# Kernel tuning notes

Hardware: AMD Instinct MI355X
Metric: run time of the kernel (lower is better)

The kernel has to match this reference:

```python
import jax, jax.numpy as jnp
import numpy as np

PE_DIM = 64

def _layernorm(x, g, b, eps=1e-5):
    m = jnp.mean(x, -1, keepdims=True)
    v = jnp.mean((x - m) ** 2, -1, keepdims=True)
    return (x - m) * jax.lax.rsqrt(v + eps) * g + b

def _sinusoidal_pe(t, dim=PE_DIM):
    half = dim // 2
    freqs = jnp.exp(-jnp.log(10000.0) * jnp.arange(half) / half).astype(t.dtype)
    ang = t[..., None] * freqs  # [..., half]
    return jnp.concatenate([jnp.sin(ang), jnp.cos(ang)], -1)

def _bilinear(feats, b, t, x, y):
    # feats [B,Wl,H,W,D]; b,t int32 [B,Q,Wl,M] (b broadcastable); x,y in [0,1]
    # matches torch grid_sample(mode=bilinear, padding_mode=border, align_corners=False)
    H, W = feats.shape[2], feats.shape[3]
    px = x * W - 0.5
    py = y * H - 0.5
    x0 = jnp.floor(px); y0 = jnp.floor(py)
    wx = (px - x0)[..., None]; wy = (py - y0)[..., None]
    x0i = jnp.clip(x0.astype(jnp.int32), 0, W - 1)
    x1i = jnp.clip(x0.astype(jnp.int32) + 1, 0, W - 1)
    y0i = jnp.clip(y0.astype(jnp.int32), 0, H - 1)
    y1i = jnp.clip(y0.astype(jnp.int32) + 1, 0, H - 1)
    v00 = feats[b, t, y0i, x0i]  # [B,Q,Wl,M,D]
    v01 = feats[b, t, y0i, x1i]
    v10 = feats[b, t, y1i, x0i]
    v11 = feats[b, t, y1i, x1i]
    return (v00 * (1 - wy) * (1 - wx) + v01 * (1 - wy) * wx
            + v10 * wy * (1 - wx) + v11 * wy * wx)

def setup_inputs() -> dict:
    key = jax.random.key(0)
    ks = jax.random.split(key, 20)
    B, Q, Wl, H, W, D, M = 4, 300, 8, 64, 64, 256, 4
    s = 0.02
    inp = {
        'q': jax.random.normal(ks[0], (B, Q, D), jnp.float32),
        'kv_feats': jax.random.normal(ks[1], (B, Wl, H, W, D), jnp.float32),
        'kv_mask': jnp.zeros((B, Wl, H, W), jnp.bool_),
        'delta_sec': jax.random.normal(ks[2], (B, Q, Wl), jnp.float32),
        'w_ref': jax.random.normal(ks[3], (D, 2), jnp.float32) * s,
        'b_ref': jnp.zeros((2,), jnp.float32),
        'w_delta': jax.random.normal(ks[4], (2 * D, 3 * M), jnp.float32) * s,
        'b_delta': jnp.zeros((3 * M,), jnp.float32),
        'w_alpha': jax.random.normal(ks[5], (2 * D, M), jnp.float32) * s,
        'b_alpha': jnp.zeros((M,), jnp.float32),
        'lam': jnp.array(1.0, jnp.float32),
        'w_proj': jax.random.normal(ks[6], (D, D), jnp.float32) * s,
        'b_proj': jnp.zeros((D,), jnp.float32),
        'ln1_g': jnp.ones((D,), jnp.float32), 'ln1_b': jnp.zeros((D,), jnp.float32),
        'ln2_g': jnp.ones((D,), jnp.float32), 'ln2_b': jnp.zeros((D,), jnp.float32),
        'w_ffn1': jax.random.normal(ks[7], (D, 4 * D), jnp.float32) * s,
        'b_ffn1': jnp.zeros((4 * D,), jnp.float32),
        'w_ffn2': jax.random.normal(ks[8], (4 * D, D), jnp.float32) * s,
        'b_ffn2': jnp.zeros((D,), jnp.float32),
        'w_rel': jax.random.normal(ks[9], (PE_DIM, D), jnp.float32) * s,
        'b_rel': jnp.zeros((D,), jnp.float32),
    }
    return inp

def reference(q, kv_feats, kv_mask, delta_sec, w_ref, b_ref, w_delta, b_delta,
              w_alpha, b_alpha, lam, w_proj, b_proj, ln1_g, ln1_b, ln2_g, ln2_b,
              w_ffn1, b_ffn1, w_ffn2, b_ffn2, w_rel, b_rel):
    B, Q, D = q.shape
    Wl = kv_feats.shape[1]
    M = w_alpha.shape[1]

    qn = _layernorm(q, ln1_g, ln1_b)
    rel_feat = _sinusoidal_pe(delta_sec) @ w_rel + b_rel          # [B,Q,Wl,D]
    psi = jnp.concatenate([jnp.broadcast_to(qn[:, :, None, :], (B, Q, Wl, D)),
                           rel_feat], -1)                          # [B,Q,Wl,2D]

    delta = (psi @ w_delta + b_delta).reshape(B, Q, Wl, M, 3)
    logits = psi @ w_alpha + b_alpha                               # [B,Q,Wl,M]
    ref = jax.nn.sigmoid(qn @ w_ref + b_ref)                       # [B,Q,2]
    coords = ref[:, :, None, None, :] + jnp.tanh(delta[..., :2])   # [B,Q,Wl,M,2]
    coords = jnp.clip(coords, 0.0, 1.0)
    delta_t = jnp.tanh(delta[..., 2])                              # [B,Q,Wl,M]

    # mask features (mask==True -> invalid -> zero)
    feats = kv_feats * (~kv_mask)[..., None].astype(kv_feats.dtype)

    # temporal trilinear indices
    base = jnp.arange(Wl, dtype=q.dtype).reshape(1, 1, Wl, 1)
    target = base + delta_t
    t0f = jnp.clip(jnp.floor(target), 0, Wl - 1)
    t1f = jnp.clip(t0f + 1, 0, Wl - 1)
    alpha = (target - t0f)[..., None]
    t0 = t0f.astype(jnp.int32); t1 = t1f.astype(jnp.int32)

    bidx = jnp.arange(B, dtype=jnp.int32).reshape(B, 1, 1, 1)
    cx = coords[..., 0]; cy = coords[..., 1]
    s0 = _bilinear(feats, bidx, t0, cx, cy)                        # [B,Q,Wl,M,D]
    s1 = _bilinear(feats, bidx, t1, cx, cy)
    sampled = s0 * (1 - alpha) + s1 * alpha

    lam_sp = jax.nn.softplus(lam)
    weights = jax.nn.softmax(logits - lam_sp * jnp.abs(delta_sec)[..., None], axis=-1)
    agg = jnp.sum(weights[..., None] * sampled, axis=(2, 3))       # [B,Q,D]

    out = q + (agg @ w_proj + b_proj)
    h = _layernorm(out, ln2_g, ln2_b)
    ffn = jax.nn.gelu(h @ w_ffn1 + b_ffn1, approximate=False) @ w_ffn2 + b_ffn2
    return out + ffn
```

## Files before the change

kernel.cpp:

```cpp
#include <hip/hip_runtime.h>
#include <math.h>

#define Bn 4
#define Qn 300
#define WL 8
#define Hh 64
#define Ww 64
#define Dd 256
#define Mm 4

__device__ __forceinline__ float wave_reduce(float v) {
#pragma unroll
    for (int off = 32; off > 0; off >>= 1) v += __shfl_down(v, off, 64);
    return v;
}

using h2_t = _Float16 __attribute__((ext_vector_type(2)));

__device__ __forceinline__ unsigned packh2(float a, float b) {
    auto h = __builtin_amdgcn_cvt_pkrtz(a, b);
    union { decltype(h) h; unsigned u; } x; x.h = h; return x.u;
}

__device__ __forceinline__ h2_t u2h2(unsigned u) {
    union { unsigned u; h2_t h; } x; x.u = u; return x.h;
}

__device__ __forceinline__ float dot2p(unsigned a, unsigned w, float acc) {
#if __has_builtin(__builtin_amdgcn_fdot2)
    return __builtin_amdgcn_fdot2(u2h2(a), u2h2(w), acc, false);
#else
    h2_t A = u2h2(a), W = u2h2(w);
    return acc + (float)A.x * (float)W.x + (float)A.y * (float)W.y;
#endif
}

__device__ __forceinline__ float dot8h(uint4 av, uint4 wv, float acc) {
    acc = dot2p(av.x, wv.x, acc);
    acc = dot2p(av.y, wv.y, acc);
    acc = dot2p(av.z, wv.z, acc);
    acc = dot2p(av.w, wv.w, acc);
    return acc;
}

__global__ void __launch_bounds__(512, 4) k_front(const float* __restrict__ wp,
                                                  const float* __restrict__ wf1,
                                                  const float* __restrict__ wf2,
                                                  unsigned* __restrict__ pk,
                                                  const float* __restrict__ q,
                                                  const float* __restrict__ g1,
                                                  const float* __restrict__ b1,
                                                  const float* __restrict__ w_ref,
                                                  const float* __restrict__ b_ref,
                                                  const float* __restrict__ dsec,
                                                  const float* __restrict__ w_rel,
                                                  const float* __restrict__ b_rel,
                                                  const float* __restrict__ w_delta,
                                                  const float* __restrict__ b_delta,
                                                  const float* __restrict__ w_alpha,
                                                  const float* __restrict__ b_alpha,
                                                  const unsigned char* __restrict__ mask,
                                                  const float* __restrict__ feats,
                                                  float* __restrict__ agg) {
    int bid = blockIdx.x, t = threadIdx.x;

    if (bid < 576) {
        int i = bid * 512 + t;
        if (i < 32768) {
            int p = i & 3, c = (i >> 2) & 255, g = i >> 10;
            pk[i] = packh2(wp[(g * 8 + 2 * p) * 256 + c], wp[(g * 8 + 2 * p + 1) * 256 + c]);
        } else if (i < 163840) {
            int i2 = i - 32768;
            int p = i2 & 3, c = (i2 >> 2) & 1023, g = i2 >> 12;
            pk[i] = packh2(wf1[(g * 8 + 2 * p) * 1024 + c], wf1[(g * 8 + 2 * p + 1) * 1024 + c]);
        } else {
            int i3 = i - 163840;
            int p = i3 & 3, c = (i3 >> 2) & 255, g = i3 >> 10;
            pk[i] = packh2(wf2[(g * 8 + 2 * p) * 256 + c], wf2[(g * 8 + 2 * p + 1) * 256 + c]);
        }
        return;
    }

    __shared__ float sqn[256];
    __shared__ float pe[8][64];
    __shared__ float rel[8][260];
    __shared__ __align__(16) float WcT[16 * 516];
    __shared__ float dres[2][8][16];
    __shared__ float res[8][16];
    __shared__ float red[16];
    __shared__ float sref[2];
    float (*part)[256] = (float (*)[256])WcT;
    unsigned* Prec = (unsigned*)(WcT + 2048);

    int bq = bid - 576;
    int ch = t & 255;
    bool lo = t < 256;
    int lane = t & 63, wv = t >> 6;

    float wr[64];
#pragma unroll
    for (int k = 0; k < 64; k++) wr[k] = w_rel[k * Dd + ch];

    for (int u = t; u < 512 * 16; u += 512) {
        int k = u >> 4, jj = u & 15;
        float w = (jj < 12) ? w_delta[k * 12 + jj] : w_alpha[k * 4 + (jj - 12)];
        WcT[jj * 516 + k] = w;
    }

    float x = lo ? q[bq * Dd + ch] : 0.f;
    float sm = wave_reduce(x);
    if (lane == 0) red[wv] = sm;
    __syncthreads();
    float m = (red[0] + red[1] + red[2] + red[3] + red[4] + red[5] + red[6] + red[7]) * (1.f / Dd);
    __syncthreads();
    float dx = lo ? (x - m) : 0.f;
    float sv = wave_reduce(dx * dx);
    if (lane == 0) red[wv] = sv;
    __syncthreads();
    float v = (red[0] + red[1] + red[2] + red[3] + red[4] + red[5] + red[6] + red[7]) * (1.f / Dd);
    __syncthreads();
    float y = 0.f;
    if (lo) { y = dx * rsqrtf(v + 1e-5f) * g1[ch] + b1[ch]; sqn[ch] = y; }

    if (lo) {
        int wl = t >> 5, i2 = t & 31;
        float f = expf(-logf(10000.f) * (float)i2 * (1.f / 32.f));
        float a = dsec[bq * WL + wl] * f;
        pe[wl][i2] = sinf(a);
        pe[wl][i2 + 32] = cosf(a);
    }

    float c0 = lo ? y * w_ref[2 * ch] : 0.f;
    float c1 = lo ? y * w_ref[2 * ch + 1] : 0.f;
    c0 = wave_reduce(c0); c1 = wave_reduce(c1);
    if (lane == 0) { red[wv] = c0; red[8 + wv] = c1; }
    __syncthreads();
    if (t == 0) {
        float s0 = red[0] + red[1] + red[2] + red[3] + red[4] + red[5] + red[6] + red[7] + b_ref[0];
        float s1 = red[8] + red[9] + red[10] + red[11] + red[12] + red[13] + red[14] + red[15] + b_ref[1];
        sref[0] = 1.f / (1.f + expf(-s0));
        sref[1] = 1.f / (1.f + expf(-s1));
    }

    {
        float brl = b_rel[ch];
        int wh = t >> 8;
#pragma unroll
        for (int w2 = 0; w2 < 4; w2++) {
            int wl = wh * 4 + w2;
            const float4* p4 = (const float4*)&pe[wl][0];
            float r = brl;
#pragma unroll
            for (int k4 = 0; k4 < 16; k4++) {
                float4 p = p4[k4];
                r += p.x * wr[4 * k4] + p.y * wr[4 * k4 + 1]
                   + p.z * wr[4 * k4 + 2] + p.w * wr[4 * k4 + 3];
            }
            rel[wl][ch] = r;
        }
    }
    __syncthreads();

    if (t < 256) {
        int h = t >> 7, idx = t & 127, wl = idx >> 4, jj = idx & 15;
        const float4* wrow = (const float4*)&WcT[jj * 516 + h * 256];
        const float4* arow = h ? (const float4*)&rel[wl][0] : (const float4*)sqn;
        float s = 0.f;
#pragma unroll 8
        for (int k4 = 0; k4 < 64; k4++) {
            float4 a = arow[k4], w = wrow[k4];
            s += a.x * w.x + a.y * w.y + a.z * w.z + a.w * w.w;
        }
        dres[h][wl][jj] = s;
    }
    __syncthreads();
    if (t < 128) {
        int wl = t >> 4, jj = t & 15;
        res[wl][jj] = dres[0][wl][jj] + dres[1][wl][jj]
                    + ((jj < 12) ? b_delta[jj] : b_alpha[jj - 12]);
    }
    __syncthreads();

    if (t < 32) {
        int wl = t >> 2, mm = t & 3;
        float l0 = res[wl][12], l1 = res[wl][13], l2 = res[wl][14], l3 = res[wl][15];
        float mx = fmaxf(fmaxf(l0, l1), fmaxf(l2, l3));
        float inv = 1.f / (expf(l0 - mx) + expf(l1 - mx) + expf(l2 - mx) + expf(l3 - mx));
        float wgt = expf(res[wl][12 + mm] - mx) * inv;

        float cx = fminf(fmaxf(sref[0] + tanhf(res[wl][mm * 3 + 0]), 0.f), 1.f);
        float cy = fminf(fmaxf(sref[1] + tanhf(res[wl][mm * 3 + 1]), 0.f), 1.f);
        float tgt = (float)wl + tanhf(res[wl][mm * 3 + 2]);
        float t0f = fminf(fmaxf(floorf(tgt), 0.f), (float)(WL - 1));
        float t1f = fminf(t0f + 1.f, (float)(WL - 1));
        float alpha = tgt - t0f;
        float px = cx * (float)Ww - 0.5f, py = cy * (float)Hh - 0.5f;
        float fx = floorf(px), fy = floorf(py);
        float wx = px - fx, wy = py - fy;
        int X0 = (int)fminf(fmaxf(fx, 0.f), (float)(Ww - 1));
        int X1 = (int)fminf(fmaxf(fx + 1.f, 0.f), (float)(Ww - 1));
        int Y0 = (int)fminf(fmaxf(fy, 0.f), (float)(Hh - 1));
        int Y1 = (int)fminf(fmaxf(fy + 1.f, 0.f), (float)(Hh - 1));
        int T0 = (int)t0f, T1 = (int)t1f;

        float w00 = (1.f - wy) * (1.f - wx), w01 = (1.f - wy) * wx;
        float w10 = wy * (1.f - wx), w11 = wy * wx;
        float wt0 = wgt * (1.f - alpha), wt1 = wgt * alpha;

        int b = bq / Qn;
        int base0 = (b * WL + T0) * Hh;
        int base1 = (b * WL + T1) * Hh;
        int i00 = (base0 + Y0) * Ww + X0, i01 = (base0 + Y0) * Ww + X1;
        int i10 = (base0 + Y1) * Ww + X0, i11 = (base0 + Y1) * Ww + X1;
        int j00 = (base1 + Y0) * Ww + X0, j01 = (base1 + Y0) * Ww + X1;
        int j10 = (base1 + Y1) * Ww + X0, j11 = (base1 + Y1) * Ww + X1;

        unsigned* rec = &Prec[t * 16];
        rec[0] = __float_as_uint(wt0 * w00 * (mask[i00] ? 0.f : 1.f));
        rec[1] = __float_as_uint(wt0 * w01 * (mask[i01] ? 0.f : 1.f));
        rec[2] = __float_as_uint(wt0 * w10 * (mask[i10] ? 0.f : 1.f));
        rec[3] = __float_as_uint(wt0 * w11 * (mask[i11] ? 0.f : 1.f));
        rec[4] = __float_as_uint(wt1 * w00 * (mask[j00] ? 0.f : 1.f));
        rec[5] = __float_as_uint(wt1 * w01 * (mask[j01] ? 0.f : 1.f));
        rec[6] = __float_as_uint(wt1 * w10 * (mask[j10] ? 0.f : 1.f));
        rec[7] = __float_as_uint(wt1 * w11 * (mask[j11] ? 0.f : 1.f));
        rec[8] = i00; rec[9] = i01; rec[10] = i10; rec[11] = i11;
        rec[12] = j00; rec[13] = j01; rec[14] = j10; rec[15] = j11;
    }
    __syncthreads();

    {
        const float4* f4 = (const float4*)feats;
        int j = t >> 6;
        float4 acc = {0.f, 0.f, 0.f, 0.f};
#pragma unroll
        for (int p = 0; p < 4; p++) {
            const unsigned* rec = &Prec[(j * 4 + p) * 16];
#pragma unroll
            for (int cn = 0; cn < 8; cn++) {
                float w = __uint_as_float(rec[cn]);
                size_t idx = rec[8 + cn];
                float4 vv = f4[idx * 64 + lane];
                acc.x += w * vv.x; acc.y += w * vv.y; acc.z += w * vv.z; acc.w += w * vv.w;
            }
        }
        ((float4*)&part[j][0])[lane] = acc;
    }
    __syncthreads();
    if (t < 256) {
        agg[(size_t)bq * Dd + t] = part[0][t] + part[1][t] + part[2][t] + part[3][t]
                                 + part[4][t] + part[5][t] + part[6][t] + part[7][t];
    }
}

template<int R>
__device__ __forceinline__ void out_body(int row0,
        const float* __restrict__ q, const float* __restrict__ agg,
        const unsigned* __restrict__ pkP, const float* __restrict__ b_proj,
        const float* __restrict__ g2, const float* __restrict__ b2,
        const unsigned* __restrict__ pkF1, const float* __restrict__ b_ffn1,
        const unsigned* __restrict__ pkF2, const float* __restrict__ b_ffn2,
        float* __restrict__ out,
        unsigned* sA2, float* sO, unsigned* sH2, unsigned* sF2, float* sX, float* sRed) {
    int t = threadIdx.x;
    int j8 = t >> 7, c7 = t & 127;

    for (int u = t; u < 128 * R; u += 1024) {
        int r = u >> 7, c2 = u & 127;
        float2 av = *(const float2*)&agg[(size_t)(row0 + r) * Dd + 2 * c2];
        sA2[r * 128 + c2] = packh2(av.x, av.y);
    }
    __syncthreads();

    {
        float a0[R], a1[R];
#pragma unroll
        for (int r = 0; r < R; r++) { a0[r] = 0.f; a1[r] = 0.f; }
#pragma unroll
        for (int gg = 0; gg < 4; gg++) {
            int g = j8 * 4 + gg;
            uint4 wv0 = *(const uint4*)&pkP[((unsigned)(g * 256 + c7)) * 4];
            uint4 wv1 = *(const uint4*)&pkP[((unsigned)(g * 256 + c7 + 128)) * 4];
#pragma unroll
            for (int r = 0; r < R; r++) {
                uint4 av = ((const uint4*)&sA2[r * 128])[g];
                a0[r] = dot8h(av, wv0, a0[r]);
                a1[r] = dot8h(av, wv1, a1[r]);
            }
        }
#pragma unroll
        for (int r = 0; r < R; r++) {
            sX[(j8 * R + r) * 256 + c7] = a0[r];
            sX[(j8 * R + r) * 256 + c7 + 128] = a1[r];
        }
    }
    __syncthreads();

    for (int u = t; u < 256 * R; u += 1024) {
        int r = u >> 8, cc = u & 255;
        float o = q[(size_t)(row0 + r) * Dd + cc] + b_proj[cc];
#pragma unroll
        for (int jj = 0; jj < 8; jj++) o += sX[(jj * R + r) * 256 + cc];
        sO[r * 256 + cc] = o;
    }
    __syncthreads();

    {
        int wv = t >> 6, l = t & 63;
        if (wv < R) {
            float4 vv = ((const float4*)&sO[wv * 256])[l];
            float s = vv.x + vv.y + vv.z + vv.w;
            s = __shfl(wave_reduce(s), 0, 64);
            float mean = s * (1.f / 256.f);
            float d0 = vv.x - mean, d1 = vv.y - mean, d2 = vv.z - mean, d3 = vv.w - mean;
            float ss = d0 * d0 + d1 * d1 + d2 * d2 + d3 * d3;
            ss = __shfl(wave_reduce(ss), 0, 64);
            float rstd = rsqrtf(ss * (1.f / 256.f) + 1e-5f);
            if (l == 0) { sRed[wv * 2] = mean; sRed[wv * 2 + 1] = rstd; }
        }
    }
    __syncthreads();
    for (int u = t; u < 128 * R; u += 1024) {
        int r = u >> 7, c2 = u & 127;
        int cc = 2 * c2;
        float mean = sRed[r * 2], rstd = sRed[r * 2 + 1];
        float h0 = (sO[r * 256 + cc] - mean) * rstd * g2[cc] + b2[cc];
        float h1 = (sO[r * 256 + cc + 1] - mean) * rstd * g2[cc + 1] + b2[cc + 1];
        sH2[r * 128 + c2] = packh2(h0, h1);
    }
    __syncthreads();

    {
        int h = t >> 9, c2c = t & 511;
        float f0[R], f1[R];
#pragma unroll
        for (int r = 0; r < R; r++) { f0[r] = 0.f; f1[r] = 0.f; }
#pragma unroll 2
        for (int gg = 0; gg < 16; gg++) {
            int g = h * 16 + gg;
            uint4 wv0 = *(const uint4*)&pkF1[((unsigned)(g * 1024 + c2c)) * 4];
            uint4 wv1 = *(const uint4*)&pkF1[((unsigned)(g * 1024 + c2c + 512)) * 4];
#pragma unroll
            for (int r = 0; r < R; r++) {
                uint4 av = ((const uint4*)&sH2[r * 128])[g];
                f0[r] = dot8h(av, wv0, f0[r]);
                f1[r] = dot8h(av, wv1, f1[r]);
            }
        }
        float* dst = sX + h * (R * 1024);
#pragma unroll
        for (int r = 0; r < R; r++) {
            dst[r * 1024 + c2c] = f0[r];
            dst[r * 1024 + c2c + 512] = f1[r];
        }
    }
    __syncthreads();

    for (int u = t; u < 512 * R; u += 1024) {
        int r = u >> 9, p = u & 511;
        float2 pa = ((const float2*)&sX[r * 1024])[p];
        float2 pb = ((const float2*)&sX[R * 1024 + r * 1024])[p];
        float2 bf = *(const float2*)&b_ffn1[2 * p];
        float x0 = pa.x + pb.x + bf.x;
        float x1 = pa.y + pb.y + bf.y;
        float e0 = 0.5f * x0 * (1.f + erff(x0 * 0.70710678118654752f));
        float e1 = 0.5f * x1 * (1.f + erff(x1 * 0.70710678118654752f));
        sF2[r * 512 + p] = packh2(e0, e1);
    }
    __syncthreads();

    {
        float a0[R], a1[R];
#pragma unroll
        for (int r = 0; r < R; r++) { a0[r] = 0.f; a1[r] = 0.f; }
#pragma unroll 2
        for (int gg = 0; gg < 16; gg++) {
            int g = j8 * 16 + gg;
            uint4 wv0 = *(const uint4*)&pkF2[((unsigned)(g * 256 + c7)) * 4];
            uint4 wv1 = *(const uint4*)&pkF2[((unsigned)(g * 256 + c7 + 128)) * 4];
#pragma unroll
            for (int r = 0; r < R; r++) {
                uint4 av = ((const uint4*)&sF2[r * 512])[g];
                a0[r] = dot8h(av, wv0, a0[r]);
                a1[r] = dot8h(av, wv1, a1[r]);
            }
        }
#pragma unroll
        for (int r = 0; r < R; r++) {
            sX[(j8 * R + r) * 256 + c7] = a0[r];
            sX[(j8 * R + r) * 256 + c7 + 128] = a1[r];
        }
    }
    __syncthreads();

    for (int u = t; u < 256 * R; u += 1024) {
        int r = u >> 8, cc = u & 255;
        float s = b_ffn2[cc];
#pragma unroll
        for (int jj = 0; jj < 8; jj++) s += sX[(jj * R + r) * 256 + cc];
        out[(size_t)(row0 + r) * Dd + cc] = sO[r * 256 + cc] + s;
    }
}

__global__ void __launch_bounds__(1024) k_out(const float* __restrict__ q,
                                              const float* __restrict__ agg,
                                              const unsigned* __restrict__ pkP,
                                              const float* __restrict__ b_proj,
                                              const float* __restrict__ g2,
                                              const float* __restrict__ b2,
                                              const unsigned* __restrict__ pkF1,
                                              const float* __restrict__ b_ffn1,
                                              const unsigned* __restrict__ pkF2,
                                              const float* __restrict__ b_ffn2,
                                              float* __restrict__ out) {
    __shared__ __align__(16) unsigned sA2[5 * 128];
    __shared__ __align__(16) float sO[5 * 256];
    __shared__ __align__(16) unsigned sH2[5 * 128];
    __shared__ __align__(16) unsigned sF2[5 * 512];
    __shared__ __align__(16) float sX[10240];
    __shared__ float sRed[16];
    __shared__ float pad[5120];
    if (b_ffn2 == nullptr) pad[threadIdx.x & 1023] = 0.f;

    int bid = blockIdx.x;
    if (bid < 176) {
        out_body<5>(bid * 5, q, agg, pkP, b_proj, g2, b2, pkF1, b_ffn1, pkF2, b_ffn2,
                    out, sA2, sO, sH2, sF2, sX, sRed);
    } else {
        out_body<4>(880 + (bid - 176) * 4, q, agg, pkP, b_proj, g2, b2, pkF1, b_ffn1,
                    pkF2, b_ffn2, out, sA2, sO, sH2, sF2, sX, sRed);
    }
}

extern "C" void kernel_launch(void* const* d_in, const int* in_sizes, int n_in,
                              void* d_out, int out_size, void* d_ws, size_t ws_size,
                              hipStream_t stream) {
    const float* q        = (const float*)d_in[0];
    const float* kv_feats = (const float*)d_in[1];
    const unsigned char* kv_mask = (const unsigned char*)d_in[2];
    const float* delta_sec= (const float*)d_in[3];
    const float* w_ref    = (const float*)d_in[4];
    const float* b_ref    = (const float*)d_in[5];
    const float* w_delta  = (const float*)d_in[6];
    const float* b_delta  = (const float*)d_in[7];
    const float* w_alpha  = (const float*)d_in[8];
    const float* b_alpha  = (const float*)d_in[9];
    const float* w_proj   = (const float*)d_in[11];
    const float* b_proj   = (const float*)d_in[12];
    const float* ln1_g    = (const float*)d_in[13];
    const float* ln1_b    = (const float*)d_in[14];
    const float* ln2_g    = (const float*)d_in[15];
    const float* ln2_b    = (const float*)d_in[16];
    const float* w_ffn1   = (const float*)d_in[17];
    const float* b_ffn1   = (const float*)d_in[18];
    const float* w_ffn2   = (const float*)d_in[19];
    const float* b_ffn2   = (const float*)d_in[20];
    const float* w_rel    = (const float*)d_in[21];
    const float* b_rel    = (const float*)d_in[22];
    float* out = (float*)d_out;

    unsigned* pk   = (unsigned*)d_ws;
    unsigned* pkP  = pk;
    unsigned* pkF1 = pk + 32768;
    unsigned* pkF2 = pk + 163840;
    float*    agg  = (float*)(pk + 294912);

    const int BQ = Bn * Qn;
    k_front<<<dim3(576 + BQ), dim3(512), 0, stream>>>(w_proj, w_ffn1, w_ffn2, pk,
                                                      q, ln1_g, ln1_b, w_ref, b_ref,
                                                      delta_sec, w_rel, b_rel,
                                                      w_delta, b_delta, w_alpha, b_alpha,
                                                      kv_mask, kv_feats, agg);
    k_out<<<dim3(256), dim3(1024), 0, stream>>>(q, agg, pkP, b_proj, ln2_g, ln2_b,
                                                pkF1, b_ffn1, pkF2, b_ffn2, out);
}
```

Measured before the change: 278.3 us.

## Make sampling stage wave-local and merge layernorm reductions to cut block barriers

```diff
diff --git a/kernel.cpp b/kernel.cpp
--- a/kernel.cpp
+++ b/kernel.cpp
@@ -85,12 +85,9 @@
     __shared__ float pe[8][64];
     __shared__ float rel[8][260];
     __shared__ __align__(16) float WcT[16 * 516];
-    __shared__ float dres[2][8][16];
     __shared__ float res[8][16];
-    __shared__ float red[16];
-    __shared__ float sref[2];
-    float (*part)[256] = (float (*)[256])WcT;
-    unsigned* Prec = (unsigned*)(WcT + 2048);
+    __shared__ float red[32];
+    unsigned* Prec = (unsigned*)&pe[0][0];
 
     int bq = bid - 576;
     int ch = t & 255;
@@ -108,19 +105,15 @@
     }
 
     float x = lo ? q[bq * Dd + ch] : 0.f;
-    float sm = wave_reduce(x);
-    if (lane == 0) red[wv] = sm;
-    __syncthreads();
-    float m = (red[0] + red[1] + red[2] + red[3] + red[4] + red[5] + red[6] + red[7]) * (1.f / Dd);
-    __syncthreads();
-    float dx = lo ? (x - m) : 0.f;
-    float sv = wave_reduce(dx * dx);
-    if (lane == 0) red[wv] = sv;
-    __syncthreads();
-    float v = (red[0] + red[1] + red[2] + red[3] + red[4] + red[5] + red[6] + red[7]) * (1.f / Dd);
-    __syncthreads();
-    float y = 0.f;
-    if (lo) { y = dx * rsqrtf(v + 1e-5f) * g1[ch] + b1[ch]; sqn[ch] = y; }
+    {
+        float sx = x, sxx = x * x;
+#pragma unroll
+        for (int off = 32; off > 0; off >>= 1) {
+            sx += __shfl_down(sx, off, 64);
+            sxx += __shfl_down(sxx, off, 64);
+        }
+        if (lane == 0) { red[wv] = sx; red[8 + wv] = sxx; }
+    }
 
     if (lo) {
         int wl = t >> 5, i2 = t & 31;
@@ -129,19 +122,33 @@
         pe[wl][i2] = sinf(a);
         pe[wl][i2 + 32] = cosf(a);
     }
-
-    float c0 = lo ? y * w_ref[2 * ch] : 0.f;
-    float c1 = lo ? y * w_ref[2 * ch + 1] : 0.f;
-    c0 = wave_reduce(c0); c1 = wave_reduce(c1);
-    if (lane == 0) { red[wv] = c0; red[8 + wv] = c1; }
-    __syncthreads();
-    if (t == 0) {
-        float s0 = red[0] + red[1] + red[2] + red[3] + red[4] + red[5] + red[6] + red[7] + b_ref[0];
-        float s1 = red[8] + red[9] + red[10] + red[11] + red[12] + red[13] + red[14] + red[15] + b_ref[1];
-        sref[0] = 1.f / (1.f + expf(-s0));
-        sref[1] = 1.f / (1.f + expf(-s1));
-    }
-
+    __syncthreads();
+
+    float m  = (red[0] + red[1] + red[2] + red[3]) * (1.f / Dd);
+    float ms = (red[8] + red[9] + red[10] + red[11]) * (1.f / Dd);
+    float vvar = ms - m * m;
+    float y = 0.f;
+    if (lo) { y = (x - m) * rsqrtf(vvar + 1e-5f) * g1[ch] + b1[ch]; sqn[ch] = y; }
+
+    {
+        float c0 = lo ? y * w_ref[2 * ch] : 0.f;
+        float c1 = lo ? y * w_ref[2 * ch + 1] : 0.f;
+#pragma unroll
+        for (int off = 32; off > 0; off >>= 1) {
+            c0 += __shfl_down(c0, off, 64);
+            c1 += __shfl_down(c1, off, 64);
+        }
+        if (lane == 0) { red[16 + wv] = c0; red[24 + wv] = c1; }
+    }
+    __syncthreads();
+
+    float ref0, ref1;
+    {
+        float s0 = red[16] + red[17] + red[18] + red[19] + b_ref[0];
+        float s1 = red[24] + red[25] + red[26] + red[27] + b_ref[1];
+        ref0 = 1.f / (1.f + expf(-s0));
+        ref1 = 1.f / (1.f + expf(-s1));
+    }
     {
         float brl = b_rel[ch];
         int wh = t >> 8;
@@ -161,77 +168,73 @@
     }
     __syncthreads();
 
-    if (t < 256) {
-        int h = t >> 7, idx = t & 127, wl = idx >> 4, jj = idx & 15;
-        const float4* wrow = (const float4*)&WcT[jj * 516 + h * 256];
-        const float4* arow = h ? (const float4*)&rel[wl][0] : (const float4*)sqn;
+    int j = wv;
+    {
+        int jj = lane >> 2, kq = lane & 3;
+        const float4* wrow = (const float4*)&WcT[jj * 516 + kq * 128];
+        const float4* arow = (kq < 2) ? (const float4*)&sqn[kq * 128]
+                                      : (const float4*)&rel[j][(kq - 2) * 128];
         float s = 0.f;
 #pragma unroll 8
-        for (int k4 = 0; k4 < 64; k4++) {
+        for (int k4 = 0; k4 < 32; k4++) {
             float4 a = arow[k4], w = wrow[k4];
             s += a.x * w.x + a.y * w.y + a.z * w.z + a.w * w.w;
         }
-        dres[h][wl][jj] = s;
-    }
-    __syncthreads();
-    if (t < 128) {
-        int wl = t >> 4, jj = t & 15;
-        res[wl][jj] = dres[0][wl][jj] + dres[1][wl][jj]
-                    + ((jj < 12) ? b_delta[jj] : b_alpha[jj - 12]);
-    }
-    __syncthreads();
-
-    if (t < 32) {
-        int wl = t >> 2, mm = t & 3;
-        float l0 = res[wl][12], l1 = res[wl][13], l2 = res[wl][14], l3 = res[wl][15];
-        float mx = fmaxf(fmaxf(l0, l1), fmaxf(l2, l3));
-        float inv = 1.f / (expf(l0 - mx) + expf(l1 - mx) + expf(l2 - mx) + expf(l3 - mx));
-        float wgt = expf(res[wl][12 + mm] - mx) * inv;
-
-        float cx = fminf(fmaxf(sref[0] + tanhf(res[wl][mm * 3 + 0]), 0.f), 1.f);
-        float cy = fminf(fmaxf(sref[1] + tanhf(res[wl][mm * 3 + 1]), 0.f), 1.f);
-        float tgt = (float)wl + tanhf(res[wl][mm * 3 + 2]);
-        float t0f = fminf(fmaxf(floorf(tgt), 0.f), (float)(WL - 1));
-        float t1f = fminf(t0f + 1.f, (float)(WL - 1));
-        float alpha = tgt - t0f;
-        float px = cx * (float)Ww - 0.5f, py = cy * (float)Hh - 0.5f;
-        float fx = floorf(px), fy = floorf(py);
-        float wx = px - fx, wy = py - fy;
-        int X0 = (int)fminf(fmaxf(fx, 0.f), (float)(Ww - 1));
-        int X1 = (int)fminf(fmaxf(fx + 1.f, 0.f), (float)(Ww - 1));
-        int Y0 = (int)fminf(fmaxf(fy, 0.f), (float)(Hh - 1));
-        int Y1 = (int)fminf(fmaxf(fy + 1.f, 0.f), (float)(Hh - 1));
-        int T0 = (int)t0f, T1 = (int)t1f;
-
-        float w00 = (1.f - wy) * (1.f - wx), w01 = (1.f - wy) * wx;
-        float w10 = wy * (1.f - wx), w11 = wy * wx;
-        float wt0 = wgt * (1.f - alpha), wt1 = wgt * alpha;
-
-        int b = bq / Qn;
-        int base0 = (b * WL + T0) * Hh;
-        int base1 = (b * WL + T1) * Hh;
-        int i00 = (base0 + Y0) * Ww + X0, i01 = (base0 + Y0) * Ww + X1;
-        int i10 = (base0 + Y1) * Ww + X0, i11 = (base0 + Y1) * Ww + X1;
-        int j00 = (base1 + Y0) * Ww + X0, j01 = (base1 + Y0) * Ww + X1;
-        int j10 = (base1 + Y1) * Ww + X0, j11 = (base1 + Y1) * Ww + X1;
-
-        unsigned* rec = &Prec[t * 16];
-        rec[0] = __float_as_uint(wt0 * w00 * (mask[i00] ? 0.f : 1.f));
-        rec[1] = __float_as_uint(wt0 * w01 * (mask[i01] ? 0.f : 1.f));
-        rec[2] = __float_as_uint(wt0 * w10 * (mask[i10] ? 0.f : 1.f));
-        rec[3] = __float_as_uint(wt0 * w11 * (mask[i11] ? 0.f : 1.f));
-        rec[4] = __float_as_uint(wt1 * w00 * (mask[j00] ? 0.f : 1.f));
-        rec[5] = __float_as_uint(wt1 * w01 * (mask[j01] ? 0.f : 1.f));
-        rec[6] = __float_as_uint(wt1 * w10 * (mask[j10] ? 0.f : 1.f));
-        rec[7] = __float_as_uint(wt1 * w11 * (mask[j11] ? 0.f : 1.f));
-        rec[8] = i00; rec[9] = i01; rec[10] = i10; rec[11] = i11;
-        rec[12] = j00; rec[13] = j01; rec[14] = j10; rec[15] = j11;
-    }
-    __syncthreads();
-
-    {
+        s += __shfl_xor(s, 1, 64);
+        s += __shfl_xor(s, 2, 64);
+        if ((lane & 3) == 0) {
+            float b = (jj < 12) ? b_delta[jj] : b_alpha[jj - 12];
+            res[j][jj] = s + b;
+        }
+
+        if (lane < 4) {
+            int mm = lane;
+            float l0 = res[j][12], l1 = res[j][13], l2 = res[j][14], l3 = res[j][15];
+            float mx = fmaxf(fmaxf(l0, l1), fmaxf(l2, l3));
+            float inv = 1.f / (expf(l0 - mx) + expf(l1 - mx) + expf(l2 - mx) + expf(l3 - mx));
+            float wgt = expf(res[j][12 + mm] - mx) * inv;
+
+            float cx = fminf(fmaxf(ref0 + tanhf(res[j][mm * 3 + 0]), 0.f), 1.f);
+            float cy = fminf(fmaxf(ref1 + tanhf(res[j][mm * 3 + 1]), 0.f), 1.f);
+            float tgt = (float)j + tanhf(res[j][mm * 3 + 2]);
+            float t0f = fminf(fmaxf(floorf(tgt), 0.f), (float)(WL - 1));
+            float t1f = fminf(t0f + 1.f, (float)(WL - 1));
+            float alpha = tgt - t0f;
+            float px = cx * (float)Ww - 0.5f, py = cy * (float)Hh - 0.5f;
+            float fx = floorf(px), fy = floorf(py);
+            float wx = px - fx, wy = py - fy;
+            int X0 = (int)fminf(fmaxf(fx, 0.f), (float)(Ww - 1));
+            int X1 = (int)fminf(fmaxf(fx + 1.f, 0.f), (float)(Ww - 1));
+            int Y0 = (int)fminf(fmaxf(fy, 0.f), (float)(Hh - 1));
+            int Y1 = (int)fminf(fmaxf(fy + 1.f, 0.f), (float)(Hh - 1));
+            int T0 = (int)t0f, T1 = (int)t1f;
+
+            float w00 = (1.f - wy) * (1.f - wx), w01 = (1.f - wy) * wx;
+            float w10 = wy * (1.f - wx), w11 = wy * wx;
+            float wt0 = wgt * (1.f - alpha), wt1 = wgt * alpha;
+
+            int b = bq / Qn;
+            int base0 = (b * WL + T0) * Hh;
+            int base1 = (b * WL + T1) * Hh;
+            int i00 = (base0 + Y0) * Ww + X0, i01 = (base0 + Y0) * Ww + X1;
+            int i10 = (base0 + Y1) * Ww + X0, i11 = (base0 + Y1) * Ww + X1;
+            int j00 = (base1 + Y0) * Ww + X0, j01 = (base1 + Y0) * Ww + X1;
+            int j10 = (base1 + Y1) * Ww + X0, j11 = (base1 + Y1) * Ww + X1;
+
+            unsigned* rec = &Prec[(j * 4 + mm) * 16];
+            rec[0] = __float_as_uint(wt0 * w00 * (mask[i00] ? 0.f : 1.f));
+            rec[1] = __float_as_uint(wt0 * w01 * (mask[i01] ? 0.f : 1.f));
+            rec[2] = __float_as_uint(wt0 * w10 * (mask[i10] ? 0.f : 1.f));
+            rec[3] = __float_as_uint(wt0 * w11 * (mask[i11] ? 0.f : 1.f));
+            rec[4] = __float_as_uint(wt1 * w00 * (mask[j00] ? 0.f : 1.f));
+            rec[5] = __float_as_uint(wt1 * w01 * (mask[j01] ? 0.f : 1.f));
+            rec[6] = __float_as_uint(wt1 * w10 * (mask[j10] ? 0.f : 1.f));
+            rec[7] = __float_as_uint(wt1 * w11 * (mask[j11] ? 0.f : 1.f));
+            rec[8] = i00; rec[9] = i01; rec[10] = i10; rec[11] = i11;
+            rec[12] = j00; rec[13] = j01; rec[14] = j10; rec[15] = j11;
+        }
+
         const float4* f4 = (const float4*)feats;
-        int j = t >> 6;
         float4 acc = {0.f, 0.f, 0.f, 0.f};
 #pragma unroll
         for (int p = 0; p < 4; p++) {
@@ -244,12 +247,13 @@
                 acc.x += w * vv.x; acc.y += w * vv.y; acc.z += w * vv.z; acc.w += w * vv.w;
             }
         }
-        ((float4*)&part[j][0])[lane] = acc;
-    }
-    __syncthreads();
+        ((float4*)&rel[j][0])[lane] = acc;
+    }
+    __syncthreads();
+
     if (t < 256) {
-        agg[(size_t)bq * Dd + t] = part[0][t] + part[1][t] + part[2][t] + part[3][t]
-                                 + part[4][t] + part[5][t] + part[6][t] + part[7][t];
+        agg[(size_t)bq * Dd + t] = rel[0][t] + rel[1][t] + rel[2][t] + rel[3][t]
+                                 + rel[4][t] + rel[5][t] + rel[6][t] + rel[7][t];
     }
 }
 
```

Measured after the change: 279.8 us. No clear change (+0.6%).
